# Kernel tuning notes

Hardware: AMD Instinct MI355X
Metric: run time of the kernel (lower is better)

Reference implementation:

```python
import jax, jax.numpy as jnp
import numpy as np

B, IN_DIM, OUT_DIM, HID, K, GH, NG = 512, 480, 400, 512, 8, 128, 32


def setup_inputs() -> dict:
    key = jax.random.key(0)
    ks = jax.random.split(key, 8)
    s = lambda fan: 1.0 / np.sqrt(fan)
    return {
        "x": jax.random.normal(ks[0], (B, IN_DIM), jnp.float32),
        "gating_idx": jnp.arange(NG, dtype=jnp.int64) + (IN_DIM - NG),
        "GW1": jax.random.normal(ks[1], (NG, GH), jnp.float32) * s(NG),
        "Gb1": jnp.zeros((GH,), jnp.float32),
        "GW2": jax.random.normal(ks[2], (GH, GH), jnp.float32) * s(GH),
        "Gb2": jnp.zeros((GH,), jnp.float32),
        "GW3": jax.random.normal(ks[3], (GH, K), jnp.float32) * s(GH),
        "Gb3": jnp.zeros((K,), jnp.float32),
        "Wk1": jax.random.normal(ks[4], (K, HID, IN_DIM), jnp.float32) * s(HID * IN_DIM) * 2.45,
        "bk1": jnp.zeros((K, HID), jnp.float32),
        "Wk2": jax.random.normal(ks[5], (K, HID, HID), jnp.float32) * s(HID * HID) * 2.45,
        "bk2": jnp.zeros((K, HID), jnp.float32),
        "Wk3": jax.random.normal(ks[6], (K, OUT_DIM, HID), jnp.float32) * s(OUT_DIM * HID) * 2.45,
        "bk3": jnp.zeros((K, OUT_DIM), jnp.float32),
    }


def _motion_layer(xin, g, Wk, bk):
    # blended per-sample weight: wi[b,o,i] = sum_k g[b,k] * Wk[k,o,i]
    # then per-sample matvec: out[b,o] = sum_i wi[b,o,i] * xin[b,i] + sum_k g[b,k]*bk[k,o]
    out = jnp.einsum('bk,koi,bi->bo', g, Wk, xin)
    return out + g @ bk


def reference(x, gating_idx, GW1, Gb1, GW2, Gb2, GW3, Gb3,
              Wk1, bk1, Wk2, bk2, Wk3, bk3):
    # gating MLP (elu, elu, linear)
    g_in = jnp.take(x, gating_idx, axis=-1)                 # [B, NG]
    h = jax.nn.elu(g_in @ GW1 + Gb1)
    h = jax.nn.elu(h @ GW2 + Gb2)
    g = h @ GW3 + Gb3                                       # [B, K] blend coefficients
    # motion network: 3 phase-blended expert layers
    y1 = jax.nn.elu(_motion_layer(x, g, Wk1, bk1))          # [B, HID]
    y2 = jax.nn.elu(_motion_layer(y1, g, Wk2, bk2))         # [B, HID]
    out = _motion_layer(y2, g, Wk3, bk3)                    # [B, OUT_DIM]
    return out
```

## Files before the change

### kernel.cpp

```cpp
#include <hip/hip_runtime.h>
#include <hip/hip_bf16.h>


typedef __hip_bfloat16 bf16;
typedef unsigned short u16;
typedef __attribute__((ext_vector_type(8))) short bf16x8;
typedef __attribute__((ext_vector_type(4))) float f32x4;

__device__ __forceinline__ float elu1(float x) { return x > 0.f ? x : expm1f(x); }

__device__ __forceinline__ u16 cvt1(float v) {
    union { bf16 h; u16 u; } c;
    c.h = __float2bfloat16(v);
    return c.u;
}

__device__ __forceinline__ void async16(const u16* g, u16* l) {
    __builtin_amdgcn_global_load_lds(
        (const __attribute__((address_space(1))) void*)g,
        (__attribute__((address_space(3))) void*)l, 16, 0, 0);
}

__global__ __launch_bounds__(256) void gating_cvt_kernel(
    const float* __restrict__ x, const int* __restrict__ idx_raw,
    const float* __restrict__ GW1, const float* __restrict__ Gb1,
    const float* __restrict__ GW2, const float* __restrict__ Gb2,
    const float* __restrict__ GW3, const float* __restrict__ Gb3,
    const float* __restrict__ Wk1, const float* __restrict__ Wk2,
    const float* __restrict__ Wk3,
    float* __restrict__ g, u16* __restrict__ xbf,
    u16* __restrict__ Wb1, u16* __restrict__ Wb2, u16* __restrict__ Wb3)
{
    __shared__ float xg[32];
    __shared__ float h1[128];
    __shared__ float h2[128];
    const int b = blockIdx.x;
    const int j = threadIdx.x;

    if (j < 32) {
        int ii;
        if (idx_raw[1] == 0) ii = (int)((const long long*)idx_raw)[j];
        else                 ii = idx_raw[j];
        if (ii < 0 || ii >= 480) ii = 448 + j;
        xg[j] = x[(size_t)b * 480 + ii];
    }
    __syncthreads();

    if (j < 128) {
        float a = Gb1[j];
        #pragma unroll
        for (int i = 0; i < 32; ++i) a += xg[i] * GW1[i * 128 + j];
        h1[j] = elu1(a);
    }
    __syncthreads();

    if (j < 128) {
        float a2 = Gb2[j];
        #pragma unroll 8
        for (int i = 0; i < 128; ++i) a2 += h1[i] * GW2[i * 128 + j];
        h2[j] = elu1(a2);
    }
    __syncthreads();

    if (j < 8) {
        float a3 = Gb3[j];
        for (int i = 0; i < 128; ++i) a3 += h2[i] * GW3[i * 8 + j];
        g[b * 8 + j] = a3;
    }

    for (int i = j; i < 480; i += 256)
        xbf[b * 480 + i] = cvt1(x[b * 480 + i]);

    #pragma unroll
    for (int jj = 0; jj < 6; ++jj) {
        const int local = jj * 256 + j;
        if (local >= 1392) break;
        const int u = b * 1392 + local;
        const float* src; u16* dst; size_t off;
        if (u < 245760)      { src = Wk1; dst = Wb1; off = (size_t)u * 8; }
        else if (u < 507904) { src = Wk2; dst = Wb2; off = (size_t)(u - 245760) * 8; }
        else                 { src = Wk3; dst = Wb3; off = (size_t)(u - 507904) * 8; }
        float4 a = *(const float4*)(src + off);
        float4 c = *(const float4*)(src + off + 4);
        union { u16 h[8]; uint4 v; } o;
        o.h[0] = cvt1(a.x); o.h[1] = cvt1(a.y); o.h[2] = cvt1(a.z); o.h[3] = cvt1(a.w);
        o.h[4] = cvt1(c.x); o.h[5] = cvt1(c.y); o.h[6] = cvt1(c.z); o.h[7] = cvt1(c.w);
        *(uint4*)(dst + off) = o.v;
    }
}

template <int IDIM, int ODIM, bool ELU, typename OutT>
__global__ __launch_bounds__(256) void layer_kernel(
    const u16*  __restrict__ A,
    const u16*  __restrict__ Wb,
    const float* __restrict__ bk,
    const float* __restrict__ g,
    OutT* __restrict__ out)
{
    constexpr int KW = 128;
    constexpr int NW = (IDIM + KW - 1) / KW;
    __shared__ u16 wbuf[2][128 * KW];

    const int ot = blockIdx.x & 31;
    const int o0 = ot * 16;
    if (o0 >= ODIM) return;
    const int m0   = (blockIdx.x >> 5) * 64;
    const int tid  = threadIdx.x;
    const int wid  = tid >> 6;
    const int lane = tid & 63;
    const int n    = lane & 15;
    const int quad = lane >> 4;
    const int w_m  = wid & 1;
    const int e0   = (wid >> 1) * 4;

    auto stage = [&](int w, u16* buf) {
        const int w0 = w * KW;
        #pragma unroll
        for (int t = 0; t < 8; ++t) {
            const int L = (wid * 8 + t) * 64 + lane;
            const int r = L >> 4, slot = L & 15;
            const int e = r >> 4, nr = r & 15;
            int koff = w0 + (slot ^ (nr & 7)) * 8;
            if (koff + 8 > IDIM) koff = IDIM - 8;
            async16(Wb + ((size_t)(e * ODIM + o0 + nr)) * IDIM + koff,
                    (u16*)buf + (size_t)(wid * 8 + t) * 512);
        }
    };

    const f32x4 zero = {0.f, 0.f, 0.f, 0.f};
    f32x4 acc[2][4] = {{zero, zero, zero, zero}, {zero, zero, zero, zero}};

    stage(0, wbuf[0]);
    __syncthreads();

    for (int w = 0; w < NW; ++w) {
        if (w + 1 < NW) stage(w + 1, wbuf[(w + 1) & 1]);

        const u16* buf = wbuf[w & 1];
        #pragma unroll
        for (int cl = 0; cl < KW / 32; ++cl) {
            const int i0 = w * KW + cl * 32;
            if (i0 >= IDIM) break;
            bf16x8 af[2];
            #pragma unroll
            for (int s = 0; s < 2; ++s)
                af[s] = *(const bf16x8*)(A + (size_t)(m0 + 16 * (2 * w_m + s) + n) * IDIM
                                           + i0 + quad * 8);
            const int cw = cl * 4 + quad;
            const int slot = (cw ^ (n & 7)) * 8;
            #pragma unroll
            for (int j = 0; j < 4; ++j) {
                bf16x8 bfr = *(const bf16x8*)(buf + ((e0 + j) * 16 + n) * KW + slot);
                acc[0][j] = __builtin_amdgcn_mfma_f32_16x16x32_bf16(af[0], bfr, acc[0][j], 0, 0, 0);
                acc[1][j] = __builtin_amdgcn_mfma_f32_16x16x32_bf16(af[1], bfr, acc[1][j], 0, 0, 0);
            }
        }
        __syncthreads();
    }

    float* part = (float*)wbuf;
    float bkv[4];
    #pragma unroll
    for (int j = 0; j < 4; ++j) bkv[j] = bk[(e0 + j) * ODIM + o0 + n];

    #pragma unroll
    for (int s = 0; s < 2; ++s) {
        #pragma unroll
        for (int r = 0; r < 4; ++r) {
            const int lrow = 16 * (2 * w_m + s) + 4 * quad + r;
            const int grow = m0 + lrow;
            float v = 0.f;
            #pragma unroll
            for (int j = 0; j < 4; ++j)
                v += g[grow * 8 + e0 + j] * (acc[s][j][r] + bkv[j]);
            part[((wid >> 1) * 64 + lrow) * 17 + n] = v;
        }
    }
    __syncthreads();

    #pragma unroll
    for (int rr = 0; rr < 4; ++rr) {
        const int lrow = 16 * wid + 4 * quad + rr;
        float v = part[lrow * 17 + n] + part[(64 + lrow) * 17 + n];
        if (ELU) v = elu1(v);
        const int grow = m0 + lrow;
        if constexpr (__hip_internal::is_same<OutT, float>::value)
            out[(size_t)grow * ODIM + o0 + n] = v;
        else
            out[(size_t)grow * ODIM + o0 + n] = cvt1(v);
    }
}

extern "C" void kernel_launch(void* const* d_in, const int* in_sizes, int n_in,
                              void* d_out, int out_size, void* d_ws, size_t ws_size,
                              hipStream_t stream)
{
    const float* x   = (const float*)d_in[0];
    const int* gidx  = (const int*)d_in[1];
    const float* GW1 = (const float*)d_in[2];
    const float* Gb1 = (const float*)d_in[3];
    const float* GW2 = (const float*)d_in[4];
    const float* Gb2 = (const float*)d_in[5];
    const float* GW3 = (const float*)d_in[6];
    const float* Gb3 = (const float*)d_in[7];
    const float* Wk1 = (const float*)d_in[8];
    const float* bk1 = (const float*)d_in[9];
    const float* Wk2 = (const float*)d_in[10];
    const float* bk2 = (const float*)d_in[11];
    const float* Wk3 = (const float*)d_in[12];
    const float* bk3 = (const float*)d_in[13];

    char* ws  = (char*)d_ws;
    float* g  = (float*)ws;
    u16* xbf  = (u16*)(ws + (64 << 10));
    u16* A1   = (u16*)(ws + (1 << 20));
    u16* A2   = (u16*)(ws + (1 << 20) + (512 << 10));
    u16* Wb1  = (u16*)(ws + (2 << 20));
    u16* Wb2  = (u16*)(ws + (6 << 20));
    u16* Wb3  = (u16*)(ws + (10 << 20));

    gating_cvt_kernel<<<512, 256, 0, stream>>>(x, gidx, GW1, Gb1, GW2, Gb2,
                                               GW3, Gb3, Wk1, Wk2, Wk3,
                                               g, xbf, Wb1, Wb2, Wb3);

    layer_kernel<480, 512, true,  u16>  <<<256, 256, 0, stream>>>(xbf, Wb1, bk1, g, A1);
    layer_kernel<512, 512, true,  u16>  <<<256, 256, 0, stream>>>(A1,  Wb2, bk2, g, A2);
    layer_kernel<512, 400, false, float><<<256, 256, 0, stream>>>(A2,  Wb3, bk3, g,
                                                                  (float*)d_out);
}
```

Before: 133.0 us.

## Fuse all stages into one cooperative kernel and overlap weight conversion with layers

Replaces the four launches with a single cooperative-groups kernel of 512 blocks that uses grid syncs between phases. The fp32-to-bf16 weight conversion is split so each layer's weights are converted during the preceding layer's phase instead of all up front. Layer tiles shrink to 32 rows by 16 outputs with a 64-wide K stage, which doubles the block count and halves LDS per block so two blocks can fit per CU. This trades launch gaps and front-loaded conversion for grid-sync cost and smaller per-block tiles, and keeps a multi-kernel fallback if the cooperative launch fails.

After: 452.9 us. +240.5%, slower.

```diff
diff --git a/kernel.cpp b/kernel.cpp
--- a/kernel.cpp
+++ b/kernel.cpp
@@ -1,5 +1,8 @@
 #include <hip/hip_runtime.h>
 #include <hip/hip_bf16.h>
+#include <hip/hip_cooperative_groups.h>
+
+namespace cg = cooperative_groups;
 
 
 typedef __hip_bfloat16 bf16;
@@ -21,21 +24,36 @@
         (__attribute__((address_space(3))) void*)l, 16, 0, 0);
 }
 
-__global__ __launch_bounds__(256) void gating_cvt_kernel(
+template <int NU>
+__device__ __forceinline__ void cvt_units(const float* __restrict__ src,
+                                          u16* __restrict__ dst, int b, int tid)
+{
+    #pragma unroll
+    for (int jj = 0; jj < (NU + 255) / 256; ++jj) {
+        const int local = jj * 256 + tid;
+        if ((NU & 255) && local >= NU) break;
+        const size_t off = ((size_t)b * NU + local) * 8;
+        float4 a = *(const float4*)(src + off);
+        float4 c = *(const float4*)(src + off + 4);
+        union { u16 h[8]; uint4 v; } o;
+        o.h[0] = cvt1(a.x); o.h[1] = cvt1(a.y); o.h[2] = cvt1(a.z); o.h[3] = cvt1(a.w);
+        o.h[4] = cvt1(c.x); o.h[5] = cvt1(c.y); o.h[6] = cvt1(c.z); o.h[7] = cvt1(c.w);
+        *(uint4*)(dst + off) = o.v;
+    }
+}
+
+__device__ __forceinline__ void phase0_body(
     const float* __restrict__ x, const int* __restrict__ idx_raw,
     const float* __restrict__ GW1, const float* __restrict__ Gb1,
     const float* __restrict__ GW2, const float* __restrict__ Gb2,
     const float* __restrict__ GW3, const float* __restrict__ Gb3,
-    const float* __restrict__ Wk1, const float* __restrict__ Wk2,
-    const float* __restrict__ Wk3,
-    float* __restrict__ g, u16* __restrict__ xbf,
-    u16* __restrict__ Wb1, u16* __restrict__ Wb2, u16* __restrict__ Wb3)
-{
-    __shared__ float xg[32];
-    __shared__ float h1[128];
-    __shared__ float h2[128];
-    const int b = blockIdx.x;
-    const int j = threadIdx.x;
+    const float* __restrict__ Wk1,
+    float* __restrict__ gout, u16* __restrict__ xbf, u16* __restrict__ Wb1,
+    u16* wbuf, int b, int j)
+{
+    float* xg = (float*)wbuf;
+    float* h1 = xg + 32;
+    float* h2 = h1 + 128;
 
     if (j < 32) {
         int ii;
@@ -65,78 +83,58 @@
     if (j < 8) {
         float a3 = Gb3[j];
         for (int i = 0; i < 128; ++i) a3 += h2[i] * GW3[i * 8 + j];
-        g[b * 8 + j] = a3;
+        gout[b * 8 + j] = a3;
     }
 
     for (int i = j; i < 480; i += 256)
         xbf[b * 480 + i] = cvt1(x[b * 480 + i]);
 
-    #pragma unroll
-    for (int jj = 0; jj < 6; ++jj) {
-        const int local = jj * 256 + j;
-        if (local >= 1392) break;
-        const int u = b * 1392 + local;
-        const float* src; u16* dst; size_t off;
-        if (u < 245760)      { src = Wk1; dst = Wb1; off = (size_t)u * 8; }
-        else if (u < 507904) { src = Wk2; dst = Wb2; off = (size_t)(u - 245760) * 8; }
-        else                 { src = Wk3; dst = Wb3; off = (size_t)(u - 507904) * 8; }
-        float4 a = *(const float4*)(src + off);
-        float4 c = *(const float4*)(src + off + 4);
-        union { u16 h[8]; uint4 v; } o;
-        o.h[0] = cvt1(a.x); o.h[1] = cvt1(a.y); o.h[2] = cvt1(a.z); o.h[3] = cvt1(a.w);
-        o.h[4] = cvt1(c.x); o.h[5] = cvt1(c.y); o.h[6] = cvt1(c.z); o.h[7] = cvt1(c.w);
-        *(uint4*)(dst + off) = o.v;
-    }
+    cvt_units<480>(Wk1, Wb1, b, j);
 }
 
 template <int IDIM, int ODIM, bool ELU, typename OutT>
-__global__ __launch_bounds__(256) void layer_kernel(
-    const u16*  __restrict__ A,
-    const u16*  __restrict__ Wb,
+__device__ __forceinline__ void layer_phase(
+    const u16* __restrict__ A,
+    const u16* __restrict__ Wb,
     const float* __restrict__ bk,
-    const float* __restrict__ g,
-    OutT* __restrict__ out)
-{
-    constexpr int KW = 128;
+    const float* __restrict__ gv,
+    OutT* __restrict__ out,
+    u16* wbuf)
+{
+    constexpr int KW = 64;
     constexpr int NW = (IDIM + KW - 1) / KW;
-    __shared__ u16 wbuf[2][128 * KW];
-
-    const int ot = blockIdx.x & 31;
-    const int o0 = ot * 16;
+    const int bid = blockIdx.x;
+    const int o0 = (bid & 31) * 16;
     if (o0 >= ODIM) return;
-    const int m0   = (blockIdx.x >> 5) * 64;
-    const int tid  = threadIdx.x;
-    const int wid  = tid >> 6;
-    const int lane = tid & 63;
-    const int n    = lane & 15;
-    const int quad = lane >> 4;
-    const int w_m  = wid & 1;
-    const int e0   = (wid >> 1) * 4;
+    const int m0  = (bid >> 5) * 32;
+    const int tid = threadIdx.x;
+    const int wid = tid >> 6, lane = tid & 63;
+    const int n = lane & 15, quad = lane >> 4;
+    const int e0 = wid * 2;
 
     auto stage = [&](int w, u16* buf) {
         const int w0 = w * KW;
         #pragma unroll
-        for (int t = 0; t < 8; ++t) {
-            const int L = (wid * 8 + t) * 64 + lane;
-            const int r = L >> 4, slot = L & 15;
+        for (int t = 0; t < 4; ++t) {
+            const int L = (wid * 4 + t) * 64 + lane;
+            const int r = L >> 3, slot = L & 7;
             const int e = r >> 4, nr = r & 15;
             int koff = w0 + (slot ^ (nr & 7)) * 8;
             if (koff + 8 > IDIM) koff = IDIM - 8;
             async16(Wb + ((size_t)(e * ODIM + o0 + nr)) * IDIM + koff,
-                    (u16*)buf + (size_t)(wid * 8 + t) * 512);
+                    buf + (size_t)(wid * 4 + t) * 512);
         }
     };
 
     const f32x4 zero = {0.f, 0.f, 0.f, 0.f};
-    f32x4 acc[2][4] = {{zero, zero, zero, zero}, {zero, zero, zero, zero}};
-
-    stage(0, wbuf[0]);
+    f32x4 acc[2][2] = {{zero, zero}, {zero, zero}};
+
+    stage(0, wbuf);
     __syncthreads();
 
     for (int w = 0; w < NW; ++w) {
-        if (w + 1 < NW) stage(w + 1, wbuf[(w + 1) & 1]);
-
-        const u16* buf = wbuf[w & 1];
+        if (w + 1 < NW) stage(w + 1, wbuf + ((w + 1) & 1) * (128 * KW));
+        const u16* buf = wbuf + (w & 1) * (128 * KW);
         #pragma unroll
         for (int cl = 0; cl < KW / 32; ++cl) {
             const int i0 = w * KW + cl * 32;
@@ -144,51 +142,114 @@
             bf16x8 af[2];
             #pragma unroll
             for (int s = 0; s < 2; ++s)
-                af[s] = *(const bf16x8*)(A + (size_t)(m0 + 16 * (2 * w_m + s) + n) * IDIM
+                af[s] = *(const bf16x8*)(A + (size_t)(m0 + 16 * s + n) * IDIM
                                            + i0 + quad * 8);
             const int cw = cl * 4 + quad;
-            const int slot = (cw ^ (n & 7)) * 8;
+            const int sl = (cw ^ (n & 7)) * 8;
             #pragma unroll
-            for (int j = 0; j < 4; ++j) {
-                bf16x8 bfr = *(const bf16x8*)(buf + ((e0 + j) * 16 + n) * KW + slot);
-                acc[0][j] = __builtin_amdgcn_mfma_f32_16x16x32_bf16(af[0], bfr, acc[0][j], 0, 0, 0);
-                acc[1][j] = __builtin_amdgcn_mfma_f32_16x16x32_bf16(af[1], bfr, acc[1][j], 0, 0, 0);
+            for (int jj = 0; jj < 2; ++jj) {
+                bf16x8 bfr = *(const bf16x8*)(buf + ((e0 + jj) * 16 + n) * KW + sl);
+                acc[0][jj] = __builtin_amdgcn_mfma_f32_16x16x32_bf16(af[0], bfr, acc[0][jj], 0, 0, 0);
+                acc[1][jj] = __builtin_amdgcn_mfma_f32_16x16x32_bf16(af[1], bfr, acc[1][jj], 0, 0, 0);
             }
         }
         __syncthreads();
     }
 
     float* part = (float*)wbuf;
-    float bkv[4];
+    float bkv[2];
     #pragma unroll
-    for (int j = 0; j < 4; ++j) bkv[j] = bk[(e0 + j) * ODIM + o0 + n];
+    for (int jj = 0; jj < 2; ++jj) bkv[jj] = bk[(e0 + jj) * ODIM + o0 + n];
 
     #pragma unroll
     for (int s = 0; s < 2; ++s) {
         #pragma unroll
         for (int r = 0; r < 4; ++r) {
-            const int lrow = 16 * (2 * w_m + s) + 4 * quad + r;
+            const int lrow = 16 * s + 4 * quad + r;
             const int grow = m0 + lrow;
             float v = 0.f;
             #pragma unroll
-            for (int j = 0; j < 4; ++j)
-                v += g[grow * 8 + e0 + j] * (acc[s][j][r] + bkv[j]);
-            part[((wid >> 1) * 64 + lrow) * 17 + n] = v;
+            for (int jj = 0; jj < 2; ++jj)
+                v += gv[grow * 8 + e0 + jj] * (acc[s][jj][r] + bkv[jj]);
+            part[(wid * 32 + lrow) * 17 + n] = v;
         }
     }
     __syncthreads();
 
     #pragma unroll
-    for (int rr = 0; rr < 4; ++rr) {
-        const int lrow = 16 * wid + 4 * quad + rr;
-        float v = part[lrow * 17 + n] + part[(64 + lrow) * 17 + n];
+    for (int rr = 0; rr < 2; ++rr) {
+        const int lrow = rr * 16 + (tid >> 4);
+        const int col  = tid & 15;
+        float v = part[lrow * 17 + col] + part[(32 + lrow) * 17 + col]
+                + part[(64 + lrow) * 17 + col] + part[(96 + lrow) * 17 + col];
         if (ELU) v = elu1(v);
-        const int grow = m0 + lrow;
         if constexpr (__hip_internal::is_same<OutT, float>::value)
-            out[(size_t)grow * ODIM + o0 + n] = v;
+            out[(size_t)(m0 + lrow) * ODIM + o0 + col] = v;
         else
-            out[(size_t)grow * ODIM + o0 + n] = cvt1(v);
-    }
+            out[(size_t)(m0 + lrow) * ODIM + o0 + col] = cvt1(v);
+    }
+}
+
+__global__ __launch_bounds__(256, 2) void fused_mann(
+    const float* __restrict__ x, const int* __restrict__ idx_raw,
+    const float* __restrict__ GW1, const float* __restrict__ Gb1,
+    const float* __restrict__ GW2, const float* __restrict__ Gb2,
+    const float* __restrict__ GW3, const float* __restrict__ Gb3,
+    const float* __restrict__ Wk1, const float* __restrict__ bk1,
+    const float* __restrict__ Wk2, const float* __restrict__ bk2,
+    const float* __restrict__ Wk3, const float* __restrict__ bk3,
+    float* __restrict__ gout, u16* __restrict__ xbf,
+    u16* __restrict__ A1, u16* __restrict__ A2,
+    u16* __restrict__ Wb1, u16* __restrict__ Wb2, u16* __restrict__ Wb3,
+    float* __restrict__ outp)
+{
+    __shared__ u16 wbuf[2][128 * 64];
+    cg::grid_group gg = cg::this_grid();
+    const int b = blockIdx.x;
+    const int j = threadIdx.x;
+
+    phase0_body(x, idx_raw, GW1, Gb1, GW2, Gb2, GW3, Gb3, Wk1,
+                gout, xbf, Wb1, &wbuf[0][0], b, j);
+    __threadfence();
+    gg.sync();
+
+    layer_phase<480, 512, true, u16>(xbf, Wb1, bk1, gout, A1, &wbuf[0][0]);
+    cvt_units<512>(Wk2, Wb2, b, j);
+    __threadfence();
+    gg.sync();
+
+    layer_phase<512, 512, true, u16>(A1, Wb2, bk2, gout, A2, &wbuf[0][0]);
+    cvt_units<400>(Wk3, Wb3, b, j);
+    __threadfence();
+    gg.sync();
+
+    layer_phase<512, 400, false, float>(A2, Wb3, bk3, gout, outp, &wbuf[0][0]);
+}
+
+__global__ __launch_bounds__(256, 2) void k_phase0(
+    const float* __restrict__ x, const int* __restrict__ idx_raw,
+    const float* __restrict__ GW1, const float* __restrict__ Gb1,
+    const float* __restrict__ GW2, const float* __restrict__ Gb2,
+    const float* __restrict__ GW3, const float* __restrict__ Gb3,
+    const float* __restrict__ Wk1,
+    float* __restrict__ gout, u16* __restrict__ xbf, u16* __restrict__ Wb1)
+{
+    __shared__ u16 wbuf[2][128 * 64];
+    phase0_body(x, idx_raw, GW1, Gb1, GW2, Gb2, GW3, Gb3, Wk1,
+                gout, xbf, Wb1, &wbuf[0][0], blockIdx.x, threadIdx.x);
+}
+
+template <int IDIM, int ODIM, bool ELU, typename OutT, int NU_NEXT>
+__global__ __launch_bounds__(256, 2) void k_layer(
+    const u16* __restrict__ A, const u16* __restrict__ Wb,
+    const float* __restrict__ bk, const float* __restrict__ gv,
+    OutT* __restrict__ out,
+    const float* __restrict__ Wnext_src, u16* __restrict__ Wnext_dst)
+{
+    __shared__ u16 wbuf[2][128 * 64];
+    layer_phase<IDIM, ODIM, ELU, OutT>(A, Wb, bk, gv, out, &wbuf[0][0]);
+    if constexpr (NU_NEXT > 0)
+        cvt_units<NU_NEXT>(Wnext_src, Wnext_dst, blockIdx.x, threadIdx.x);
 }
 
 extern "C" void kernel_launch(void* const* d_in, const int* in_sizes, int n_in,
@@ -218,13 +279,27 @@
     u16* Wb1  = (u16*)(ws + (2 << 20));
     u16* Wb2  = (u16*)(ws + (6 << 20));
     u16* Wb3  = (u16*)(ws + (10 << 20));
-
-    gating_cvt_kernel<<<512, 256, 0, stream>>>(x, gidx, GW1, Gb1, GW2, Gb2,
-                                               GW3, Gb3, Wk1, Wk2, Wk3,
-                                               g, xbf, Wb1, Wb2, Wb3);
-
-    layer_kernel<480, 512, true,  u16>  <<<256, 256, 0, stream>>>(xbf, Wb1, bk1, g, A1);
-    layer_kernel<512, 512, true,  u16>  <<<256, 256, 0, stream>>>(A1,  Wb2, bk2, g, A2);
-    layer_kernel<512, 400, false, float><<<256, 256, 0, stream>>>(A2,  Wb3, bk3, g,
-                                                                  (float*)d_out);
-}
+    float* outp = (float*)d_out;
+
+    void* params[] = {
+        (void*)&x,   (void*)&gidx, (void*)&GW1, (void*)&Gb1,
+        (void*)&GW2, (void*)&Gb2,  (void*)&GW3, (void*)&Gb3,
+        (void*)&Wk1, (void*)&bk1,  (void*)&Wk2, (void*)&bk2,
+        (void*)&Wk3, (void*)&bk3,
+        (void*)&g,   (void*)&xbf,  (void*)&A1,  (void*)&A2,
+        (void*)&Wb1, (void*)&Wb2,  (void*)&Wb3, (void*)&outp
+    };
+    hipError_t err = hipLaunchCooperativeKernel(fused_mann, dim3(512), dim3(256),
+                                                params, 0u, stream);
+    if (err != hipSuccess) {
+        k_phase0<<<512, 256, 0, stream>>>(x, gidx, GW1, Gb1, GW2, Gb2,
+                                          GW3, Gb3, Wk1, g, xbf, Wb1);
+        k_layer<480, 512, true,  u16,  512><<<512, 256, 0, stream>>>(
+            xbf, Wb1, bk1, g, A1, Wk2, Wb2);
+        k_layer<512, 512, true,  u16,  400><<<512, 256, 0, stream>>>(
+            A1,  Wb2, bk2, g, A2, Wk3, Wb3);
+        k_layer<512, 400, false, float, 0><<<512, 256, 0, stream>>>(
+            A2,  Wb3, bk3, g, (float*)d_out, (const float*)nullptr, (u16*)nullptr);
+    }
+    (void)outp;
+}
```

## Distribute expert weight bf16 conversion into preceding layer kernels

Applied to the files above, without the earlier changes.

Moves conversion of Wk2 and Wk3 from the gating kernel into the tail of the layer-1 and layer-2 kernels, so each conversion happens just before its weights are needed. This shortens the gating kernel and puts the conversion memory traffic inside kernels that otherwise have spare bandwidth. The risk is longer layer kernels, because the conversion runs after each GEMM rather than overlapping with it inside a block.

Result: no change. 133.4 us (+0.3%).

```diff
diff --git a/kernel.cpp b/kernel.cpp
--- a/kernel.cpp
+++ b/kernel.cpp
@@ -19,6 +19,24 @@
     __builtin_amdgcn_global_load_lds(
         (const __attribute__((address_space(1))) void*)g,
         (__attribute__((address_space(3))) void*)l, 16, 0, 0);
+}
+
+template <int NU>
+__device__ __forceinline__ void cvt_units(const float* __restrict__ src,
+                                          u16* __restrict__ dst, int b, int tid)
+{
+    #pragma unroll
+    for (int jj = 0; jj < (NU + 255) / 256; ++jj) {
+        const int local = jj * 256 + tid;
+        if ((NU & 255) && local >= NU) break;
+        const size_t off = ((size_t)b * NU + local) * 8;
+        float4 a = *(const float4*)(src + off);
+        float4 c = *(const float4*)(src + off + 4);
+        union { u16 h[8]; uint4 v; } o;
+        o.h[0] = cvt1(a.x); o.h[1] = cvt1(a.y); o.h[2] = cvt1(a.z); o.h[3] = cvt1(a.w);
+        o.h[4] = cvt1(c.x); o.h[5] = cvt1(c.y); o.h[6] = cvt1(c.z); o.h[7] = cvt1(c.w);
+        *(uint4*)(dst + off) = o.v;
+    }
 }
 
 __global__ __launch_bounds__(256) void gating_cvt_kernel(
@@ -26,10 +44,8 @@
     const float* __restrict__ GW1, const float* __restrict__ Gb1,
     const float* __restrict__ GW2, const float* __restrict__ Gb2,
     const float* __restrict__ GW3, const float* __restrict__ Gb3,
-    const float* __restrict__ Wk1, const float* __restrict__ Wk2,
-    const float* __restrict__ Wk3,
-    float* __restrict__ g, u16* __restrict__ xbf,
-    u16* __restrict__ Wb1, u16* __restrict__ Wb2, u16* __restrict__ Wb3)
+    const float* __restrict__ Wk1,
+    float* __restrict__ g, u16* __restrict__ xbf, u16* __restrict__ Wb1)
 {
     __shared__ float xg[32];
     __shared__ float h1[128];
@@ -71,31 +87,17 @@
     for (int i = j; i < 480; i += 256)
         xbf[b * 480 + i] = cvt1(x[b * 480 + i]);
 
-    #pragma unroll
-    for (int jj = 0; jj < 6; ++jj) {
-        const int local = jj * 256 + j;
-        if (local >= 1392) break;
-        const int u = b * 1392 + local;
-        const float* src; u16* dst; size_t off;
-        if (u < 245760)      { src = Wk1; dst = Wb1; off = (size_t)u * 8; }
-        else if (u < 507904) { src = Wk2; dst = Wb2; off = (size_t)(u - 245760) * 8; }
-        else                 { src = Wk3; dst = Wb3; off = (size_t)(u - 507904) * 8; }
-        float4 a = *(const float4*)(src + off);
-        float4 c = *(const float4*)(src + off + 4);
-        union { u16 h[8]; uint4 v; } o;
-        o.h[0] = cvt1(a.x); o.h[1] = cvt1(a.y); o.h[2] = cvt1(a.z); o.h[3] = cvt1(a.w);
-        o.h[4] = cvt1(c.x); o.h[5] = cvt1(c.y); o.h[6] = cvt1(c.z); o.h[7] = cvt1(c.w);
-        *(uint4*)(dst + off) = o.v;
-    }
-}
-
-template <int IDIM, int ODIM, bool ELU, typename OutT>
+    cvt_units<480>(Wk1, Wb1, b, j);
+}
+
+template <int IDIM, int ODIM, bool ELU, typename OutT, int NU_NEXT>
 __global__ __launch_bounds__(256) void layer_kernel(
     const u16*  __restrict__ A,
     const u16*  __restrict__ Wb,
     const float* __restrict__ bk,
     const float* __restrict__ g,
-    OutT* __restrict__ out)
+    OutT* __restrict__ out,
+    const float* __restrict__ Wnext_src, u16* __restrict__ Wnext_dst)
 {
     constexpr int KW = 128;
     constexpr int NW = (IDIM + KW - 1) / KW;
@@ -103,7 +105,7 @@
 
     const int ot = blockIdx.x & 31;
     const int o0 = ot * 16;
-    if (o0 >= ODIM) return;
+    if (o0 < ODIM) {
     const int m0   = (blockIdx.x >> 5) * 64;
     const int tid  = threadIdx.x;
     const int wid  = tid >> 6;
@@ -189,6 +191,10 @@
         else
             out[(size_t)grow * ODIM + o0 + n] = cvt1(v);
     }
+    }
+
+    if constexpr (NU_NEXT > 0)
+        cvt_units<NU_NEXT>(Wnext_src, Wnext_dst, blockIdx.x, threadIdx.x);
 }
 
 extern "C" void kernel_launch(void* const* d_in, const int* in_sizes, int n_in,
@@ -220,11 +226,11 @@
     u16* Wb3  = (u16*)(ws + (10 << 20));
 
     gating_cvt_kernel<<<512, 256, 0, stream>>>(x, gidx, GW1, Gb1, GW2, Gb2,
-                                               GW3, Gb3, Wk1, Wk2, Wk3,
-                                               g, xbf, Wb1, Wb2, Wb3);
-
-    layer_kernel<480, 512, true,  u16>  <<<256, 256, 0, stream>>>(xbf, Wb1, bk1, g, A1);
-    layer_kernel<512, 512, true,  u16>  <<<256, 256, 0, stream>>>(A1,  Wb2, bk2, g, A2);
-    layer_kernel<512, 400, false, float><<<256, 256, 0, stream>>>(A2,  Wb3, bk3, g,
-                                                                  (float*)d_out);
-}
+                                               GW3, Gb3, Wk1, g, xbf, Wb1);
+    layer_kernel<480, 512, true,  u16,  1024><<<256, 256, 0, stream>>>(
+        xbf, Wb1, bk1, g, A1, Wk2, Wb2);
+    layer_kernel<512, 512, true,  u16,  800><<<256, 256, 0, stream>>>(
+        A1,  Wb2, bk2, g, A2, Wk3, Wb3);
+    layer_kernel<512, 400, false, float, 0><<<256, 256, 0, stream>>>(
+        A2,  Wb3, bk3, g, (float*)d_out, (const float*)nullptr, (u16*)nullptr);
+}
```

## Fuse three expert layers into one kernel with per-row-group flag barriers

Applied to the files above, without the earlier changes.

Replaces the three separate layer kernel launches with a single kernel of 256 blocks that runs all three blended layers in turn. Between layers, the 32 blocks that share a batch row group wait on a global atomic counter, which the gating kernel resets. This removes two kernel launch gaps and their drain and fill tails. In exchange it relies on all 256 blocks being resident at the same time and adds spin-wait and fence overhead.

After: 213.0 us. 1.6x slower.

```diff
diff --git a/kernel.cpp b/kernel.cpp
--- a/kernel.cpp
+++ b/kernel.cpp
@@ -29,13 +29,16 @@
     const float* __restrict__ Wk1, const float* __restrict__ Wk2,
     const float* __restrict__ Wk3,
     float* __restrict__ g, u16* __restrict__ xbf,
-    u16* __restrict__ Wb1, u16* __restrict__ Wb2, u16* __restrict__ Wb3)
+    u16* __restrict__ Wb1, u16* __restrict__ Wb2, u16* __restrict__ Wb3,
+    int* __restrict__ ctr)
 {
     __shared__ float xg[32];
     __shared__ float h1[128];
     __shared__ float h2[128];
     const int b = blockIdx.x;
     const int j = threadIdx.x;
+
+    if (b == 0 && j < 16) ctr[j] = 0;
 
     if (j < 32) {
         int ii;
@@ -90,16 +93,16 @@
 }
 
 template <int IDIM, int ODIM, bool ELU, typename OutT>
-__global__ __launch_bounds__(256) void layer_kernel(
+__device__ __forceinline__ void layer_body(
     const u16*  __restrict__ A,
     const u16*  __restrict__ Wb,
     const float* __restrict__ bk,
     const float* __restrict__ g,
-    OutT* __restrict__ out)
+    OutT* __restrict__ out,
+    u16* lds)
 {
     constexpr int KW = 128;
     constexpr int NW = (IDIM + KW - 1) / KW;
-    __shared__ u16 wbuf[2][128 * KW];
 
     const int ot = blockIdx.x & 31;
     const int o0 = ot * 16;
@@ -123,20 +126,20 @@
             int koff = w0 + (slot ^ (nr & 7)) * 8;
             if (koff + 8 > IDIM) koff = IDIM - 8;
             async16(Wb + ((size_t)(e * ODIM + o0 + nr)) * IDIM + koff,
-                    (u16*)buf + (size_t)(wid * 8 + t) * 512);
+                    buf + (size_t)(wid * 8 + t) * 512);
         }
     };
 
     const f32x4 zero = {0.f, 0.f, 0.f, 0.f};
     f32x4 acc[2][4] = {{zero, zero, zero, zero}, {zero, zero, zero, zero}};
 
-    stage(0, wbuf[0]);
+    stage(0, lds);
     __syncthreads();
 
     for (int w = 0; w < NW; ++w) {
-        if (w + 1 < NW) stage(w + 1, wbuf[(w + 1) & 1]);
-
-        const u16* buf = wbuf[w & 1];
+        if (w + 1 < NW) stage(w + 1, lds + ((w + 1) & 1) * (128 * KW));
+
+        const u16* buf = lds + (w & 1) * (128 * KW);
         #pragma unroll
         for (int cl = 0; cl < KW / 32; ++cl) {
             const int i0 = w * KW + cl * 32;
@@ -158,7 +161,7 @@
         __syncthreads();
     }
 
-    float* part = (float*)wbuf;
+    float* part = (float*)lds;
     float bkv[4];
     #pragma unroll
     for (int j = 0; j < 4; ++j) bkv[j] = bk[(e0 + j) * ODIM + o0 + n];
@@ -189,6 +192,41 @@
         else
             out[(size_t)grow * ODIM + o0 + n] = cvt1(v);
     }
+}
+
+__device__ __forceinline__ void flag_sync(int* ctr, int m, int tid)
+{
+    __threadfence();
+    __syncthreads();
+    if (tid == 0) {
+        atomicAdd(&ctr[m], 1);
+        while (atomicAdd(&ctr[m], 0) < 32)
+            __builtin_amdgcn_s_sleep(2);
+    }
+    __syncthreads();
+    __threadfence();
+}
+
+__global__ __launch_bounds__(256) void k_layers(
+    const u16*  __restrict__ xbf,
+    const u16*  __restrict__ Wb1, const float* __restrict__ bk1,
+    const u16*  __restrict__ Wb2, const float* __restrict__ bk2,
+    const u16*  __restrict__ Wb3, const float* __restrict__ bk3,
+    const float* __restrict__ g,
+    u16* __restrict__ A1, u16* __restrict__ A2,
+    float* __restrict__ out, int* __restrict__ ctr)
+{
+    __shared__ u16 wbuf[2][128 * 128];
+    const int tid = threadIdx.x;
+    const int m   = blockIdx.x >> 5;
+
+    layer_body<480, 512, true,  u16>(xbf, Wb1, bk1, g, A1, &wbuf[0][0]);
+    flag_sync(ctr, m, tid);
+
+    layer_body<512, 512, true,  u16>(A1, Wb2, bk2, g, A2, &wbuf[0][0]);
+    flag_sync(ctr + 8, m, tid);
+
+    layer_body<512, 400, false, float>(A2, Wb3, bk3, g, out, &wbuf[0][0]);
 }
 
 extern "C" void kernel_launch(void* const* d_in, const int* in_sizes, int n_in,
@@ -212,6 +250,7 @@
 
     char* ws  = (char*)d_ws;
     float* g  = (float*)ws;
+    int* ctr  = (int*)(ws + (32 << 10));
     u16* xbf  = (u16*)(ws + (64 << 10));
     u16* A1   = (u16*)(ws + (1 << 20));
     u16* A2   = (u16*)(ws + (1 << 20) + (512 << 10));
@@ -221,10 +260,7 @@
 
     gating_cvt_kernel<<<512, 256, 0, stream>>>(x, gidx, GW1, Gb1, GW2, Gb2,
                                                GW3, Gb3, Wk1, Wk2, Wk3,
-                                               g, xbf, Wb1, Wb2, Wb3);
-
-    layer_kernel<480, 512, true,  u16>  <<<256, 256, 0, stream>>>(xbf, Wb1, bk1, g, A1);
-    layer_kernel<512, 512, true,  u16>  <<<256, 256, 0, stream>>>(A1,  Wb2, bk2, g, A2);
-    layer_kernel<512, 400, false, float><<<256, 256, 0, stream>>>(A2,  Wb3, bk3, g,
-                                                                  (float*)d_out);
-}
+                                               g, xbf, Wb1, Wb2, Wb3, ctr);
+    k_layers<<<256, 256, 0, stream>>>(xbf, Wb1, bk1, Wb2, bk2, Wb3, bk3,
+                                      g, A1, A2, (float*)d_out, ctr);
+}
```
